# Performance work log

Hardware: AMD Instinct MI355X
Metric: run time of the kernel (lower is better)

## Reference

```python
import jax, jax.numpy as jnp
import numpy as np

STAGE_NUM = 5
BETA = 1.0
EPS = 1e-6


def _em_refine(cls, proto):
    # cls: [b, d]; proto: [k, d]. Matches torch einsum('bd,bkd->bk') with
    # batch-replicated prototypes == cls @ proto.T (no (b,k,d) materialization).
    p = proto
    for _ in range(STAGE_NUM):
        r = jax.nn.softmax(cls @ p.T, axis=1)          # [b, k]
        p = r.T @ cls                                   # [k, d]
        p = p / (jnp.linalg.norm(p, axis=1, keepdims=True) + EPS)
    return p


def setup_inputs() -> dict:
    key = jax.random.key(0)
    k1, k2 = jax.random.split(key)
    b, d, k = 8192, 1024, 512
    cls = jax.random.normal(k1, (b, d), dtype=jnp.float32)
    proto = jax.random.normal(k2, (k, d), dtype=jnp.float32)
    # __init__ normalizes prototypes to unit norm (with 1e-6 in denominator)
    proto = proto / (1e-6 + jnp.linalg.norm(proto, axis=1, keepdims=True))
    return {"cls": cls, "prototypes": proto}


def reference(cls, prototypes):
    # EM loop runs under torch.no_grad() -> stop_gradient here.
    new_proto = jax.lax.stop_gradient(_em_refine(cls, prototypes))  # [k, d]
    dot = cls @ new_proto.T                                          # [b, k]
    r = jax.nn.softmax(dot, axis=1)
    z_recon = r @ new_proto                                          # [b, d]
    z_out = BETA * z_recon + cls
    return (r, z_out)
```

## Files before the change

kernel.cpp:

```cpp
#include <hip/hip_runtime.h>

typedef short v8s __attribute__((ext_vector_type(8)));
typedef _Float16 v8h __attribute__((ext_vector_type(8)));
typedef float v4f __attribute__((ext_vector_type(4)));

typedef __attribute__((address_space(1))) const void* as1_void_cp;
typedef __attribute__((address_space(3))) void* as3_void_p;

__device__ __forceinline__ unsigned short f2bf(float x) {
  union { float f; unsigned int u; } v; v.f = x;
  unsigned int r = v.u + 0x7fffu + ((v.u >> 16) & 1u);
  return (unsigned short)(r >> 16);
}
__device__ __forceinline__ float bf2f(unsigned short h) {
  union { unsigned int u; float f; } v; v.u = ((unsigned int)h) << 16;
  return v.f;
}
__device__ __forceinline__ unsigned short f2h(float x) {
  _Float16 h = (_Float16)x;
  return __builtin_bit_cast(unsigned short, h);
}

struct B3 { int x, y, z; };
__device__ __forceinline__ B3 xcd_swizzle() {
  const int gx = gridDim.x, gy = gridDim.y;
  const int nwg = gx * gy * gridDim.z;
  int flat = blockIdx.x + gx * (blockIdx.y + gy * blockIdx.z);
  if ((nwg & 7) == 0) flat = (flat & 7) * (nwg >> 3) + (flat >> 3);
  B3 b;
  b.x = flat % gx;
  b.y = (flat / gx) % gy;
  b.z = flat / (gx * gy);
  return b;
}

template <bool ADD, bool F16>
__global__ __launch_bounds__(256) void gemm_bt(
    const unsigned short* __restrict__ A, const unsigned short* __restrict__ B,
    float* __restrict__ C, const float* __restrict__ Cadd,
    int N, int lda, int ldb, int klen, size_t csplit) {
  __shared__ __align__(16) unsigned short As[2][128 * 64];
  __shared__ __align__(16) unsigned short Bs[2][128 * 64];
  const int tid = threadIdx.x;
  const B3 bid = xcd_swizzle();
  const int bn = bid.x * 128, bm = bid.y * 128;
  const int k0 = bid.z * klen;
  float* Cp = C + (size_t)bid.z * csplit;

  const unsigned short* ag0 = A + (size_t)(bm + (tid >> 2)) * lda + ((tid & 3) << 3) + k0;
  const unsigned short* ag1 = ag0 + (size_t)64 * lda;
  const unsigned short* bg0 = B + (size_t)(bn + (tid >> 2)) * ldb + ((tid & 3) << 3) + k0;
  const unsigned short* bg1 = bg0 + (size_t)64 * ldb;

  const int lane = tid & 63;
  const int q = lane >> 4, m15 = lane & 15;
  const int w = tid >> 6;
  const int wr = (w >> 1) * 64, wc = (w & 1) * 64;

  v4f acc[4][4];
#pragma unroll
  for (int i = 0; i < 4; ++i)
#pragma unroll
    for (int j = 0; j < 4; ++j) acc[i][j] = 0.f;

  auto stage = [&](int kk, int b) {
    unsigned short* al = As[b] + tid * 8;
    unsigned short* bl = Bs[b] + tid * 8;
    __builtin_amdgcn_global_load_lds((as1_void_cp)(ag0 + kk), (as3_void_p)al, 16, 0, 0);
    __builtin_amdgcn_global_load_lds((as1_void_cp)(ag1 + kk), (as3_void_p)(al + 2048), 16, 0, 0);
    __builtin_amdgcn_global_load_lds((as1_void_cp)(ag0 + kk + 32), (as3_void_p)(al + 4096), 16, 0, 0);
    __builtin_amdgcn_global_load_lds((as1_void_cp)(ag1 + kk + 32), (as3_void_p)(al + 6144), 16, 0, 0);
    __builtin_amdgcn_global_load_lds((as1_void_cp)(bg0 + kk), (as3_void_p)bl, 16, 0, 0);
    __builtin_amdgcn_global_load_lds((as1_void_cp)(bg1 + kk), (as3_void_p)(bl + 2048), 16, 0, 0);
    __builtin_amdgcn_global_load_lds((as1_void_cp)(bg0 + kk + 32), (as3_void_p)(bl + 4096), 16, 0, 0);
    __builtin_amdgcn_global_load_lds((as1_void_cp)(bg1 + kk + 32), (as3_void_p)(bl + 6144), 16, 0, 0);
  };

  const int nt = klen >> 6;
  stage(0, 0);
  if (nt > 1) stage(64, 1);
  for (int t = 0; t < nt; ++t) {
    if (t + 1 < nt)
      asm volatile("s_waitcnt vmcnt(8)" ::: "memory");
    else
      asm volatile("s_waitcnt vmcnt(0)" ::: "memory");
    __builtin_amdgcn_s_barrier();
    const unsigned short* Ab = As[t & 1];
    const unsigned short* Bb = Bs[t & 1];
#pragma unroll
    for (int h = 0; h < 2; ++h) {
      v8s af[4], bf[4];
#pragma unroll
      for (int i = 0; i < 4; ++i)
        af[i] = *(const v8s*)(Ab + h * 4096 + (wr + i * 16 + m15) * 32 + q * 8);
#pragma unroll
      for (int j = 0; j < 4; ++j)
        bf[j] = *(const v8s*)(Bb + h * 4096 + (wc + j * 16 + m15) * 32 + q * 8);
#pragma unroll
      for (int i = 0; i < 4; ++i)
#pragma unroll
        for (int j = 0; j < 4; ++j) {
          if constexpr (F16)
            acc[i][j] = __builtin_amdgcn_mfma_f32_16x16x32_f16(
                __builtin_bit_cast(v8h, af[i]), __builtin_bit_cast(v8h, bf[j]), acc[i][j], 0, 0, 0);
          else
            acc[i][j] = __builtin_amdgcn_mfma_f32_16x16x32_bf16(af[i], bf[j], acc[i][j], 0, 0, 0);
        }
    }
    if (t + 2 < nt) {
      __builtin_amdgcn_s_barrier();
      stage((t + 2) << 6, t & 1);
    }
  }

#pragma unroll
  for (int i = 0; i < 4; ++i) {
#pragma unroll
    for (int j = 0; j < 4; ++j) {
      const int col = bn + wc + j * 16 + m15;
#pragma unroll
      for (int rr = 0; rr < 4; ++rr) {
        const int row = bm + wr + i * 16 + q * 4 + rr;
        const size_t idx = (size_t)row * N + col;
        float v = acc[i][j][rr];
        if (ADD) v += Cadd[idx];
        Cp[idx] = v;
      }
    }
  }
}

__global__ __launch_bounds__(256) void gemm_bt3(
    const unsigned short* __restrict__ Ah, const unsigned short* __restrict__ Al,
    const unsigned short* __restrict__ Bh, const unsigned short* __restrict__ Bl,
    float* __restrict__ C, int N, int lda, int ldb, int klen, size_t csplit) {
  __shared__ __align__(16) unsigned short Ash[2][128 * 32];
  __shared__ __align__(16) unsigned short Asl[2][128 * 32];
  __shared__ __align__(16) unsigned short Bsh[2][128 * 32];
  __shared__ __align__(16) unsigned short Bsl[2][128 * 32];
  const int tid = threadIdx.x;
  const B3 bid = xcd_swizzle();
  const int bn = bid.x * 128, bm = bid.y * 128;
  const int k0 = bid.z * klen;
  float* Cp = C + (size_t)bid.z * csplit;

  const size_t aoff = (size_t)(bm + (tid >> 2)) * lda + ((tid & 3) << 3) + k0;
  const size_t boff = (size_t)(bn + (tid >> 2)) * ldb + ((tid & 3) << 3) + k0;
  const unsigned short* agh0 = Ah + aoff;
  const unsigned short* agh1 = agh0 + (size_t)64 * lda;
  const unsigned short* agl0 = Al + aoff;
  const unsigned short* agl1 = agl0 + (size_t)64 * lda;
  const unsigned short* bgh0 = Bh + boff;
  const unsigned short* bgh1 = bgh0 + (size_t)64 * ldb;
  const unsigned short* bgl0 = Bl + boff;
  const unsigned short* bgl1 = bgl0 + (size_t)64 * ldb;

  const int lane = tid & 63;
  const int q = lane >> 4, m15 = lane & 15;
  const int w = tid >> 6;
  const int wr = (w >> 1) * 64, wc = (w & 1) * 64;

  v4f acc[4][4];
#pragma unroll
  for (int i = 0; i < 4; ++i)
#pragma unroll
    for (int j = 0; j < 4; ++j) acc[i][j] = 0.f;

  auto stage = [&](int kk, int b) {
    __builtin_amdgcn_global_load_lds((as1_void_cp)(agh0 + kk), (as3_void_p)(Ash[b] + tid * 8), 16, 0, 0);
    __builtin_amdgcn_global_load_lds((as1_void_cp)(agh1 + kk), (as3_void_p)(Ash[b] + 2048 + tid * 8), 16, 0, 0);
    __builtin_amdgcn_global_load_lds((as1_void_cp)(agl0 + kk), (as3_void_p)(Asl[b] + tid * 8), 16, 0, 0);
    __builtin_amdgcn_global_load_lds((as1_void_cp)(agl1 + kk), (as3_void_p)(Asl[b] + 2048 + tid * 8), 16, 0, 0);
    __builtin_amdgcn_global_load_lds((as1_void_cp)(bgh0 + kk), (as3_void_p)(Bsh[b] + tid * 8), 16, 0, 0);
    __builtin_amdgcn_global_load_lds((as1_void_cp)(bgh1 + kk), (as3_void_p)(Bsh[b] + 2048 + tid * 8), 16, 0, 0);
    __builtin_amdgcn_global_load_lds((as1_void_cp)(bgl0 + kk), (as3_void_p)(Bsl[b] + tid * 8), 16, 0, 0);
    __builtin_amdgcn_global_load_lds((as1_void_cp)(bgl1 + kk), (as3_void_p)(Bsl[b] + 2048 + tid * 8), 16, 0, 0);
  };

  const int nt = klen >> 5;
  stage(0, 0);
  if (nt > 1) stage(32, 1);
  for (int t = 0; t < nt; ++t) {
    if (t + 1 < nt)
      asm volatile("s_waitcnt vmcnt(8)" ::: "memory");
    else
      asm volatile("s_waitcnt vmcnt(0)" ::: "memory");
    __builtin_amdgcn_s_barrier();
    const int b = t & 1;
    v8s afh[4], afl[4], bfh[4], bfl[4];
#pragma unroll
    for (int i = 0; i < 4; ++i) {
      const int ro = (wr + i * 16 + m15) * 32 + q * 8;
      afh[i] = *(const v8s*)(Ash[b] + ro);
      afl[i] = *(const v8s*)(Asl[b] + ro);
    }
#pragma unroll
    for (int j = 0; j < 4; ++j) {
      const int ro = (wc + j * 16 + m15) * 32 + q * 8;
      bfh[j] = *(const v8s*)(Bsh[b] + ro);
      bfl[j] = *(const v8s*)(Bsl[b] + ro);
    }
#pragma unroll
    for (int i = 0; i < 4; ++i)
#pragma unroll
      for (int j = 0; j < 4; ++j) {
        acc[i][j] = __builtin_amdgcn_mfma_f32_16x16x32_bf16(afh[i], bfh[j], acc[i][j], 0, 0, 0);
        acc[i][j] = __builtin_amdgcn_mfma_f32_16x16x32_bf16(afh[i], bfl[j], acc[i][j], 0, 0, 0);
        acc[i][j] = __builtin_amdgcn_mfma_f32_16x16x32_bf16(afl[i], bfh[j], acc[i][j], 0, 0, 0);
      }
    if (t + 2 < nt) {
      __builtin_amdgcn_s_barrier();
      stage((t + 2) << 5, b);
    }
  }

#pragma unroll
  for (int i = 0; i < 4; ++i) {
#pragma unroll
    for (int j = 0; j < 4; ++j) {
      const int col = bn + wc + j * 16 + m15;
#pragma unroll
      for (int rr = 0; rr < 4; ++rr) {
        const int row = bm + wr + i * 16 + q * 4 + rr;
        Cp[(size_t)row * N + col] = acc[i][j][rr];
      }
    }
  }
}

__global__ __launch_bounds__(256) void cast_split_transpose_cls(
    const float* __restrict__ cls,
    unsigned short* __restrict__ ch, unsigned short* __restrict__ cl,
    unsigned short* __restrict__ cTh, unsigned short* __restrict__ cTl,
    unsigned short* __restrict__ cg, unsigned short* __restrict__ cTg) {
  __shared__ unsigned short th[64][72];
  __shared__ unsigned short tl[64][72];
  const int d0 = blockIdx.x * 64, b0 = blockIdx.y * 64;
  const int t = threadIdx.x;
#pragma unroll
  for (int i = 0; i < 4; ++i) {
    int flat = t + i * 256;
    int bl_ = flat >> 4;
    int dl = (flat & 15) << 2;
    float4 v = *(const float4*)(cls + (size_t)(b0 + bl_) * 1024 + d0 + dl);
    ushort4 h, l, g;
    h.x = f2bf(v.x); l.x = f2bf(v.x - bf2f(h.x)); g.x = f2h(bf2f(h.x) + bf2f(l.x));
    h.y = f2bf(v.y); l.y = f2bf(v.y - bf2f(h.y)); g.y = f2h(bf2f(h.y) + bf2f(l.y));
    h.z = f2bf(v.z); l.z = f2bf(v.z - bf2f(h.z)); g.z = f2h(bf2f(h.z) + bf2f(l.z));
    h.w = f2bf(v.w); l.w = f2bf(v.w - bf2f(h.w)); g.w = f2h(bf2f(h.w) + bf2f(l.w));
    *(ushort4*)(ch + (size_t)(b0 + bl_) * 1024 + d0 + dl) = h;
    *(ushort4*)(cl + (size_t)(b0 + bl_) * 1024 + d0 + dl) = l;
    *(ushort4*)(cg + (size_t)(b0 + bl_) * 1024 + d0 + dl) = g;
    th[bl_][dl] = h.x; th[bl_][dl + 1] = h.y; th[bl_][dl + 2] = h.z; th[bl_][dl + 3] = h.w;
    tl[bl_][dl] = l.x; tl[bl_][dl + 1] = l.y; tl[bl_][dl + 2] = l.z; tl[bl_][dl + 3] = l.w;
  }
  __syncthreads();
#pragma unroll
  for (int i = 0; i < 4; ++i) {
    int flat = t + i * 256;
    int dl = flat >> 4;
    int bl_ = (flat & 15) << 2;
    ushort4 h = make_ushort4(th[bl_][dl], th[bl_ + 1][dl], th[bl_ + 2][dl], th[bl_ + 3][dl]);
    ushort4 l = make_ushort4(tl[bl_][dl], tl[bl_ + 1][dl], tl[bl_ + 2][dl], tl[bl_ + 3][dl]);
    ushort4 g;
    g.x = f2h(bf2f(h.x) + bf2f(l.x));
    g.y = f2h(bf2f(h.y) + bf2f(l.y));
    g.z = f2h(bf2f(h.z) + bf2f(l.z));
    g.w = f2h(bf2f(h.w) + bf2f(l.w));
    *(ushort4*)(cTh + (size_t)(d0 + dl) * 8192 + b0 + bl_) = h;
    *(ushort4*)(cTl + (size_t)(d0 + dl) * 8192 + b0 + bl_) = l;
    *(ushort4*)(cTg + (size_t)(d0 + dl) * 8192 + b0 + bl_) = g;
  }
}

__global__ __launch_bounds__(256) void split_f32(const float* __restrict__ in,
                                                 unsigned short* __restrict__ hi,
                                                 unsigned short* __restrict__ lo) {
  const size_t i = (size_t)(blockIdx.x * blockDim.x + threadIdx.x) * 4;
  float4 v = *(const float4*)(in + i);
  ushort4 h, l;
  h.x = f2bf(v.x); l.x = f2bf(v.x - bf2f(h.x));
  h.y = f2bf(v.y); l.y = f2bf(v.y - bf2f(h.y));
  h.z = f2bf(v.z); l.z = f2bf(v.z - bf2f(h.z));
  h.w = f2bf(v.w); l.w = f2bf(v.w - bf2f(h.w));
  *(ushort4*)(hi + i) = h;
  *(ushort4*)(lo + i) = l;
}

template <bool HILO>
__global__ __launch_bounds__(512) void rowsoftmax_T(
    const float* __restrict__ SP0, const float* __restrict__ SP1,
    unsigned short* __restrict__ rTh, unsigned short* __restrict__ rTl) {
  __shared__ __align__(16) unsigned short th[32 * 520];
  __shared__ __align__(16) unsigned short tl[HILO ? 32 * 520 : 8];
  const int t = threadIdx.x;
  const int lane = t & 63, w = t >> 6;
  const int b0 = blockIdx.x * 32;
#pragma unroll
  for (int k = 0; k < 4; ++k) {
    const int bl = w * 4 + k;
    const int row = b0 + bl;
    const size_t off = (size_t)row * 512 + lane * 8;
    float4 v0 = *(const float4*)(SP0 + off);
    float4 v1 = *(const float4*)(SP0 + off + 4);
    float4 u0 = *(const float4*)(SP1 + off);
    float4 u1 = *(const float4*)(SP1 + off + 4);
    float e[8];
    e[0] = v0.x + u0.x; e[1] = v0.y + u0.y; e[2] = v0.z + u0.z; e[3] = v0.w + u0.w;
    e[4] = v1.x + u1.x; e[5] = v1.y + u1.y; e[6] = v1.z + u1.z; e[7] = v1.w + u1.w;
    float m = fmaxf(fmaxf(fmaxf(e[0], e[1]), fmaxf(e[2], e[3])),
                    fmaxf(fmaxf(e[4], e[5]), fmaxf(e[6], e[7])));
    for (int o = 32; o; o >>= 1) m = fmaxf(m, __shfl_xor(m, o));
    float s = 0.f;
#pragma unroll
    for (int i = 0; i < 8; ++i) { e[i] = __expf(e[i] - m); s += e[i]; }
    for (int o = 32; o; o >>= 1) s += __shfl_xor(s, o);
    const float inv = 1.f / s;
    unsigned short ph[8], pl[8];
#pragma unroll
    for (int i = 0; i < 8; ++i) {
      const float r = e[i] * inv;
      if constexpr (HILO) {
        ph[i] = f2bf(r);
        pl[i] = f2bf(r - bf2f(ph[i]));
      } else {
        ph[i] = f2h(r);
      }
    }
    *(v8s*)&th[bl * 520 + lane * 8] = *(v8s*)ph;
    if constexpr (HILO) *(v8s*)&tl[bl * 520 + lane * 8] = *(v8s*)pl;
  }
  __syncthreads();
  const int c = t;
  unsigned short uh[32];
#pragma unroll
  for (int b = 0; b < 32; ++b) uh[b] = th[b * 520 + c];
#pragma unroll
  for (int q = 0; q < 4; ++q)
    *(v8s*)(rTh + (size_t)c * 8192 + b0 + q * 8) = *(v8s*)&uh[q * 8];
  if constexpr (HILO) {
    unsigned short ul[32];
#pragma unroll
    for (int b = 0; b < 32; ++b) ul[b] = tl[b * 520 + c];
#pragma unroll
    for (int q = 0; q < 4; ++q)
      *(v8s*)(rTl + (size_t)c * 8192 + b0 + q * 8) = *(v8s*)&ul[q * 8];
  }
}

__global__ __launch_bounds__(256) void softmax_rows(const float* __restrict__ SP0,
                                                    const float* __restrict__ SP1,
                                                    float* __restrict__ r_out,
                                                    unsigned short* __restrict__ r_g) {
  const int w = threadIdx.x >> 6, lane = threadIdx.x & 63;
  const int row = blockIdx.x * 4 + w;
  const size_t off = (size_t)row * 512 + lane * 8;
  float4 v0 = *(const float4*)(SP0 + off);
  float4 v1 = *(const float4*)(SP0 + off + 4);
  float4 u0 = *(const float4*)(SP1 + off);
  float4 u1 = *(const float4*)(SP1 + off + 4);
  v0.x += u0.x; v0.y += u0.y; v0.z += u0.z; v0.w += u0.w;
  v1.x += u1.x; v1.y += u1.y; v1.z += u1.z; v1.w += u1.w;
  float m = fmaxf(fmaxf(fmaxf(v0.x, v0.y), fmaxf(v0.z, v0.w)),
                  fmaxf(fmaxf(v1.x, v1.y), fmaxf(v1.z, v1.w)));
  for (int off2 = 32; off2; off2 >>= 1) m = fmaxf(m, __shfl_xor(m, off2));
  float e0 = __expf(v0.x - m), e1 = __expf(v0.y - m), e2 = __expf(v0.z - m), e3 = __expf(v0.w - m);
  float e4 = __expf(v1.x - m), e5 = __expf(v1.y - m), e6 = __expf(v1.z - m), e7 = __expf(v1.w - m);
  float s = e0 + e1 + e2 + e3 + e4 + e5 + e6 + e7;
  for (int off2 = 32; off2; off2 >>= 1) s += __shfl_xor(s, off2);
  const float inv = 1.f / s;
  e0 *= inv; e1 *= inv; e2 *= inv; e3 *= inv; e4 *= inv; e5 *= inv; e6 *= inv; e7 *= inv;
  float* rp = r_out + off;
  *(float4*)rp = make_float4(e0, e1, e2, e3);
  *(float4*)(rp + 4) = make_float4(e4, e5, e6, e7);
  unsigned short* bp = r_g + off;
  *(ushort4*)bp = make_ushort4(f2h(e0), f2h(e1), f2h(e2), f2h(e3));
  *(ushort4*)(bp + 4) = make_ushort4(f2h(e4), f2h(e5), f2h(e6), f2h(e7));
}

__global__ __launch_bounds__(256) void reduce_normalize(const float* __restrict__ Pp,
                                                        unsigned short* __restrict__ pg,
                                                        unsigned short* __restrict__ pTg) {
  __shared__ float red[4];
  const int c = blockIdx.x, t = threadIdx.x;
  float ax = 0.f, ay = 0.f, az = 0.f, aw = 0.f;
#pragma unroll
  for (int s = 0; s < 16; ++s) {
    const float4 v = *(const float4*)(Pp + ((size_t)s * 512 + c) * 1024 + t * 4);
    ax += v.x; ay += v.y; az += v.z; aw += v.w;
  }
  float ss = ax * ax + ay * ay + az * az + aw * aw;
  for (int off = 32; off; off >>= 1) ss += __shfl_xor(ss, off);
  const int w = t >> 6, lane = t & 63;
  if (!lane) red[w] = ss;
  __syncthreads();
  const float tot = red[0] + red[1] + red[2] + red[3];
  const float scale = 1.f / (sqrtf(tot) + 1e-6f);
  ax *= scale; ay *= scale; az *= scale; aw *= scale;
  *(ushort4*)(pg + (size_t)c * 1024 + t * 4) =
      make_ushort4(f2h(ax), f2h(ay), f2h(az), f2h(aw));
  pTg[(size_t)(t * 4 + 0) * 512 + c] = f2h(ax);
  pTg[(size_t)(t * 4 + 1) * 512 + c] = f2h(ay);
  pTg[(size_t)(t * 4 + 2) * 512 + c] = f2h(az);
  pTg[(size_t)(t * 4 + 3) * 512 + c] = f2h(aw);
}

extern "C" void kernel_launch(void* const* d_in, const int* in_sizes, int n_in,
                              void* d_out, int out_size, void* d_ws, size_t ws_size,
                              hipStream_t stream) {
  const float* cls = (const float*)d_in[0];
  const float* proto = (const float*)d_in[1];
  float* out_r = (float*)d_out;
  float* out_z = out_r + (size_t)8192 * 512;

  char* w = (char*)d_ws;
  unsigned short* cls_h = (unsigned short*)w; w += (size_t)8192 * 1024 * 2;
  unsigned short* cls_l = (unsigned short*)w; w += (size_t)8192 * 1024 * 2;
  unsigned short* clsT_h = (unsigned short*)w; w += (size_t)1024 * 8192 * 2;
  unsigned short* clsT_l = (unsigned short*)w; w += (size_t)1024 * 8192 * 2;
  unsigned short* cls_g = (unsigned short*)w; w += (size_t)8192 * 1024 * 2;
  unsigned short* clsT_g = (unsigned short*)w; w += (size_t)1024 * 8192 * 2;
  unsigned short* p_h = (unsigned short*)w; w += (size_t)512 * 1024 * 2;
  unsigned short* p_l = (unsigned short*)w; w += (size_t)512 * 1024 * 2;
  unsigned short* p_g = (unsigned short*)w; w += (size_t)512 * 1024 * 2;
  unsigned short* pT_g = (unsigned short*)w; w += (size_t)1024 * 512 * 2;
  unsigned short* rT_h = (unsigned short*)w; w += (size_t)512 * 8192 * 2;
  unsigned short* rT_l = (unsigned short*)w; w += (size_t)512 * 8192 * 2;
  float* SP = (float*)w;
  float* SP1 = SP + (size_t)8192 * 512;

  cast_split_transpose_cls<<<dim3(16, 128), 256, 0, stream>>>(
      cls, cls_h, cls_l, clsT_h, clsT_l, cls_g, clsT_g);
  split_f32<<<512, 256, 0, stream>>>(proto, p_h, p_l);

  gemm_bt3<<<dim3(4, 64, 2), 256, 0, stream>>>(cls_h, cls_l, p_h, p_l, SP,
                                               512, 1024, 1024, 512,
                                               (size_t)8192 * 512);
  rowsoftmax_T<true><<<256, 512, 0, stream>>>(SP, SP1, rT_h, rT_l);
  gemm_bt3<<<dim3(8, 4, 16), 256, 0, stream>>>(rT_h, rT_l, clsT_h, clsT_l, SP,
                                               1024, 8192, 8192, 512,
                                               (size_t)512 * 1024);
  reduce_normalize<<<512, 256, 0, stream>>>(SP, p_g, pT_g);

  for (int it = 0; it < 4; ++it) {
    gemm_bt<false, true><<<dim3(4, 64, 2), 256, 0, stream>>>(cls_g, p_g, SP, nullptr,
                                                             512, 1024, 1024, 512,
                                                             (size_t)8192 * 512);
    rowsoftmax_T<false><<<256, 512, 0, stream>>>(SP, SP1, rT_h, nullptr);
    gemm_bt<false, true><<<dim3(8, 4, 16), 256, 0, stream>>>(rT_h, clsT_g, SP, nullptr,
                                                             1024, 8192, 8192, 512,
                                                             (size_t)512 * 1024);
    reduce_normalize<<<512, 256, 0, stream>>>(SP, p_g, pT_g);
  }

  gemm_bt<false, true><<<dim3(4, 64, 2), 256, 0, stream>>>(cls_g, p_g, SP, nullptr,
                                                           512, 1024, 1024, 512,
                                                           (size_t)8192 * 512);
  softmax_rows<<<2048, 256, 0, stream>>>(SP, SP1, out_r, rT_h);
  gemm_bt<true, true><<<dim3(8, 64, 1), 256, 0, stream>>>(rT_h, pT_g, out_z, cls,
                                                          1024, 512, 512, 512, 0);
}
```

Before: 446.1 us.

## Fuse score GEMM with row softmax and transpose into one kernel

Adds a kernel in which each block computes a 32-row by 512-column score tile with f16 MFMA and then applies the row softmax in registers. It writes the transposed f16 responsibilities directly, or in the final pass the fp32 r output plus the row-major f16 copy. This replaces the split-K score GEMM, its fp32 partial-sum round trip and the separate softmax kernel in the last five EM stages. The risk is that only 256 blocks run, with a large LDS footprint (about 136 KB), which limits occupancy and parallelism compared with the old split-K launch.

Result: slower. 471.2 us (+5.6%).

```diff
diff --git a/kernel.cpp b/kernel.cpp
--- a/kernel.cpp
+++ b/kernel.cpp
@@ -225,6 +225,173 @@
         Cp[(size_t)row * N + col] = acc[i][j][rr];
       }
     }
+  }
+}
+
+template <bool FINAL>
+__global__ __launch_bounds__(256) void s_softmax_fused(
+    const unsigned short* __restrict__ A,
+    const unsigned short* __restrict__ B,
+    unsigned short* __restrict__ rT,
+    float* __restrict__ r_out,
+    unsigned short* __restrict__ r_row) {
+  __shared__ __align__(16) unsigned short As[2][32 * 64];
+  __shared__ __align__(16) unsigned short Bs[2][512 * 64];
+  __shared__ float redm[4][32];
+  __shared__ float reds[4][32];
+  const int tid = threadIdx.x;
+  const int lane = tid & 63;
+  const int wv = tid >> 6;
+  const int q = lane >> 4, m15 = lane & 15;
+  const int wc = wv * 128;
+  const int b0 = blockIdx.x * 32;
+
+  const int srow = tid >> 3, scol = (tid & 7) << 3;
+  const unsigned short* ag = A + (size_t)(b0 + srow) * 1024 + scol;
+  const unsigned short* bg = B + (size_t)srow * 1024 + scol;
+
+  auto stage = [&](int kk, int b) {
+    __builtin_amdgcn_global_load_lds((as1_void_cp)(ag + kk), (as3_void_p)(As[b] + tid * 8), 16, 0, 0);
+#pragma unroll
+    for (int s = 0; s < 16; ++s)
+      __builtin_amdgcn_global_load_lds((as1_void_cp)(bg + (size_t)s * 32 * 1024 + kk),
+                                       (as3_void_p)(Bs[b] + s * 2048 + tid * 8), 16, 0, 0);
+  };
+
+  v4f acc[2][8];
+#pragma unroll
+  for (int i = 0; i < 2; ++i)
+#pragma unroll
+    for (int j = 0; j < 8; ++j) acc[i][j] = 0.f;
+
+  stage(0, 0);
+  stage(64, 1);
+  for (int t = 0; t < 16; ++t) {
+    if (t < 15)
+      asm volatile("s_waitcnt vmcnt(17)" ::: "memory");
+    else
+      asm volatile("s_waitcnt vmcnt(0)" ::: "memory");
+    __builtin_amdgcn_s_barrier();
+    const unsigned short* Ab = As[t & 1];
+    const unsigned short* Bb = Bs[t & 1];
+#pragma unroll
+    for (int h = 0; h < 2; ++h) {
+      v8s af[2], bf[8];
+#pragma unroll
+      for (int i = 0; i < 2; ++i)
+        af[i] = *(const v8s*)(Ab + (i * 16 + m15) * 64 + h * 32 + q * 8);
+#pragma unroll
+      for (int j = 0; j < 8; ++j)
+        bf[j] = *(const v8s*)(Bb + (wc + j * 16 + m15) * 64 + h * 32 + q * 8);
+#pragma unroll
+      for (int i = 0; i < 2; ++i)
+#pragma unroll
+        for (int j = 0; j < 8; ++j)
+          acc[i][j] = __builtin_amdgcn_mfma_f32_16x16x32_f16(
+              __builtin_bit_cast(v8h, af[i]), __builtin_bit_cast(v8h, bf[j]), acc[i][j], 0, 0, 0);
+    }
+    if (t + 2 < 16) {
+      __builtin_amdgcn_s_barrier();
+      stage((t + 2) << 6, t & 1);
+    }
+  }
+
+  float mx[2][4];
+#pragma unroll
+  for (int i = 0; i < 2; ++i)
+#pragma unroll
+    for (int rr = 0; rr < 4; ++rr) {
+      float m = acc[i][0][rr];
+#pragma unroll
+      for (int j = 1; j < 8; ++j) m = fmaxf(m, acc[i][j][rr]);
+      m = fmaxf(m, __shfl_xor(m, 1));
+      m = fmaxf(m, __shfl_xor(m, 2));
+      m = fmaxf(m, __shfl_xor(m, 4));
+      m = fmaxf(m, __shfl_xor(m, 8));
+      mx[i][rr] = m;
+    }
+  if (m15 == 0) {
+#pragma unroll
+    for (int i = 0; i < 2; ++i)
+#pragma unroll
+      for (int rr = 0; rr < 4; ++rr) redm[wv][i * 16 + q * 4 + rr] = mx[i][rr];
+  }
+  __syncthreads();
+#pragma unroll
+  for (int i = 0; i < 2; ++i)
+#pragma unroll
+    for (int rr = 0; rr < 4; ++rr) {
+      const int row = i * 16 + q * 4 + rr;
+      mx[i][rr] = fmaxf(fmaxf(redm[0][row], redm[1][row]),
+                        fmaxf(redm[2][row], redm[3][row]));
+    }
+
+  float sm[2][4];
+#pragma unroll
+  for (int i = 0; i < 2; ++i)
+#pragma unroll
+    for (int rr = 0; rr < 4; ++rr) {
+      float s = 0.f;
+#pragma unroll
+      for (int j = 0; j < 8; ++j) {
+        const float e = __expf(acc[i][j][rr] - mx[i][rr]);
+        acc[i][j][rr] = e;
+        s += e;
+      }
+      s += __shfl_xor(s, 1);
+      s += __shfl_xor(s, 2);
+      s += __shfl_xor(s, 4);
+      s += __shfl_xor(s, 8);
+      sm[i][rr] = s;
+    }
+  if (m15 == 0) {
+#pragma unroll
+    for (int i = 0; i < 2; ++i)
+#pragma unroll
+      for (int rr = 0; rr < 4; ++rr) reds[wv][i * 16 + q * 4 + rr] = sm[i][rr];
+  }
+  __syncthreads();
+#pragma unroll
+  for (int i = 0; i < 2; ++i)
+#pragma unroll
+    for (int rr = 0; rr < 4; ++rr) {
+      const int row = i * 16 + q * 4 + rr;
+      sm[i][rr] = 1.f / (reds[0][row] + reds[1][row] + reds[2][row] + reds[3][row]);
+    }
+
+  unsigned short* th = (unsigned short*)&Bs[0][0];
+#pragma unroll
+  for (int i = 0; i < 2; ++i)
+#pragma unroll
+    for (int j = 0; j < 8; ++j)
+#pragma unroll
+      for (int rr = 0; rr < 4; ++rr) {
+        const float v = acc[i][j][rr] * sm[i][rr];
+        const int row = i * 16 + q * 4 + rr;
+        const int col = wc + j * 16 + m15;
+        th[row * 520 + col] = f2h(v);
+        if constexpr (FINAL) r_out[(size_t)(b0 + row) * 512 + col] = v;
+      }
+  __syncthreads();
+
+  if constexpr (!FINAL) {
+#pragma unroll
+    for (int cc = 0; cc < 2; ++cc) {
+      const int c = tid + cc * 256;
+      unsigned short uh[32];
+#pragma unroll
+      for (int b = 0; b < 32; ++b) uh[b] = th[b * 520 + c];
+#pragma unroll
+      for (int u = 0; u < 4; ++u)
+        *(v8s*)(rT + (size_t)c * 8192 + b0 + u * 8) = *(v8s*)&uh[u * 8];
+    }
+  } else {
+    const int row = tid >> 3;
+    const int c0 = (tid & 7) * 64;
+#pragma unroll
+    for (int u = 0; u < 8; ++u)
+      *(v8s*)(r_row + (size_t)(b0 + row) * 512 + c0 + u * 8) =
+          *(const v8s*)&th[row * 520 + c0 + u * 8];
   }
 }
 
@@ -348,36 +515,6 @@
   }
 }
 
-__global__ __launch_bounds__(256) void softmax_rows(const float* __restrict__ SP0,
-                                                    const float* __restrict__ SP1,
-                                                    float* __restrict__ r_out,
-                                                    unsigned short* __restrict__ r_g) {
-  const int w = threadIdx.x >> 6, lane = threadIdx.x & 63;
-  const int row = blockIdx.x * 4 + w;
-  const size_t off = (size_t)row * 512 + lane * 8;
-  float4 v0 = *(const float4*)(SP0 + off);
-  float4 v1 = *(const float4*)(SP0 + off + 4);
-  float4 u0 = *(const float4*)(SP1 + off);
-  float4 u1 = *(const float4*)(SP1 + off + 4);
-  v0.x += u0.x; v0.y += u0.y; v0.z += u0.z; v0.w += u0.w;
-  v1.x += u1.x; v1.y += u1.y; v1.z += u1.z; v1.w += u1.w;
-  float m = fmaxf(fmaxf(fmaxf(v0.x, v0.y), fmaxf(v0.z, v0.w)),
-                  fmaxf(fmaxf(v1.x, v1.y), fmaxf(v1.z, v1.w)));
-  for (int off2 = 32; off2; off2 >>= 1) m = fmaxf(m, __shfl_xor(m, off2));
-  float e0 = __expf(v0.x - m), e1 = __expf(v0.y - m), e2 = __expf(v0.z - m), e3 = __expf(v0.w - m);
-  float e4 = __expf(v1.x - m), e5 = __expf(v1.y - m), e6 = __expf(v1.z - m), e7 = __expf(v1.w - m);
-  float s = e0 + e1 + e2 + e3 + e4 + e5 + e6 + e7;
-  for (int off2 = 32; off2; off2 >>= 1) s += __shfl_xor(s, off2);
-  const float inv = 1.f / s;
-  e0 *= inv; e1 *= inv; e2 *= inv; e3 *= inv; e4 *= inv; e5 *= inv; e6 *= inv; e7 *= inv;
-  float* rp = r_out + off;
-  *(float4*)rp = make_float4(e0, e1, e2, e3);
-  *(float4*)(rp + 4) = make_float4(e4, e5, e6, e7);
-  unsigned short* bp = r_g + off;
-  *(ushort4*)bp = make_ushort4(f2h(e0), f2h(e1), f2h(e2), f2h(e3));
-  *(ushort4*)(bp + 4) = make_ushort4(f2h(e4), f2h(e5), f2h(e6), f2h(e7));
-}
-
 __global__ __launch_bounds__(256) void reduce_normalize(const float* __restrict__ Pp,
                                                         unsigned short* __restrict__ pg,
                                                         unsigned short* __restrict__ pTg) {
@@ -443,20 +580,14 @@
   reduce_normalize<<<512, 256, 0, stream>>>(SP, p_g, pT_g);
 
   for (int it = 0; it < 4; ++it) {
-    gemm_bt<false, true><<<dim3(4, 64, 2), 256, 0, stream>>>(cls_g, p_g, SP, nullptr,
-                                                             512, 1024, 1024, 512,
-                                                             (size_t)8192 * 512);
-    rowsoftmax_T<false><<<256, 512, 0, stream>>>(SP, SP1, rT_h, nullptr);
+    s_softmax_fused<false><<<256, 256, 0, stream>>>(cls_g, p_g, rT_h, nullptr, nullptr);
     gemm_bt<false, true><<<dim3(8, 4, 16), 256, 0, stream>>>(rT_h, clsT_g, SP, nullptr,
                                                              1024, 8192, 8192, 512,
                                                              (size_t)512 * 1024);
     reduce_normalize<<<512, 256, 0, stream>>>(SP, p_g, pT_g);
   }
 
-  gemm_bt<false, true><<<dim3(4, 64, 2), 256, 0, stream>>>(cls_g, p_g, SP, nullptr,
-                                                           512, 1024, 1024, 512,
-                                                           (size_t)8192 * 512);
-  softmax_rows<<<2048, 256, 0, stream>>>(SP, SP1, out_r, rT_h);
+  s_softmax_fused<true><<<256, 256, 0, stream>>>(cls_g, p_g, nullptr, out_r, rT_h);
   gemm_bt<true, true><<<dim3(8, 64, 1), 256, 0, stream>>>(rT_h, pT_g, out_z, cls,
                                                           1024, 512, 512, 512, 0);
 }
```

## Add 64x128 K64 fp16 GEMM and drop split-K in EM iterations

Applied to the files above, without the earlier changes.

Adds gemm_bt64, an fp16 MFMA GEMM with a 64x128 output tile and a 64-wide K stage, double-buffered through global_load_lds. In the four low-precision EM iterations and the final score GEMM, it replaces the 128x128 split-K=2 score GEMM with a 64-row tile and no split. The update GEMM drops from split-K 16 to 8. This removes the second partial-sum buffer read in the softmax kernels and halves the partial reads in reduce_normalize, at the cost of smaller tiles with lower per-block reuse.

Measured after the change: 436.9 us. 2.1% less time.

```diff
diff --git a/kernel.cpp b/kernel.cpp
--- a/kernel.cpp
+++ b/kernel.cpp
@@ -125,6 +125,90 @@
         float v = acc[i][j][rr];
         if (ADD) v += Cadd[idx];
         Cp[idx] = v;
+      }
+    }
+  }
+}
+
+__global__ __launch_bounds__(256) void gemm_bt64(
+    const unsigned short* __restrict__ A, const unsigned short* __restrict__ B,
+    float* __restrict__ C, int N, int lda, int ldb, int klen, size_t csplit) {
+  __shared__ __align__(16) unsigned short As[2][64 * 64];
+  __shared__ __align__(16) unsigned short Bs[2][128 * 64];
+  const int tid = threadIdx.x;
+  const B3 bid = xcd_swizzle();
+  const int bn = bid.x * 128, bm = bid.y * 64;
+  const int k0 = bid.z * klen;
+  float* Cp = C + (size_t)bid.z * csplit;
+
+  const unsigned short* ag0 = A + (size_t)(bm + (tid >> 2)) * lda + ((tid & 3) << 3) + k0;
+  const unsigned short* bg0 = B + (size_t)(bn + (tid >> 2)) * ldb + ((tid & 3) << 3) + k0;
+  const unsigned short* bg1 = bg0 + (size_t)64 * ldb;
+
+  const int lane = tid & 63;
+  const int q = lane >> 4, m15 = lane & 15;
+  const int w = tid >> 6;
+  const int wr = (w >> 1) * 32, wc = (w & 1) * 64;
+
+  v4f acc[2][4];
+#pragma unroll
+  for (int i = 0; i < 2; ++i)
+#pragma unroll
+    for (int j = 0; j < 4; ++j) acc[i][j] = 0.f;
+
+  auto stage = [&](int kk, int b) {
+    unsigned short* al = As[b] + tid * 8;
+    unsigned short* bl = Bs[b] + tid * 8;
+    __builtin_amdgcn_global_load_lds((as1_void_cp)(ag0 + kk), (as3_void_p)al, 16, 0, 0);
+    __builtin_amdgcn_global_load_lds((as1_void_cp)(ag0 + kk + 32), (as3_void_p)(al + 2048), 16, 0, 0);
+    __builtin_amdgcn_global_load_lds((as1_void_cp)(bg0 + kk), (as3_void_p)bl, 16, 0, 0);
+    __builtin_amdgcn_global_load_lds((as1_void_cp)(bg1 + kk), (as3_void_p)(bl + 2048), 16, 0, 0);
+    __builtin_amdgcn_global_load_lds((as1_void_cp)(bg0 + kk + 32), (as3_void_p)(bl + 4096), 16, 0, 0);
+    __builtin_amdgcn_global_load_lds((as1_void_cp)(bg1 + kk + 32), (as3_void_p)(bl + 6144), 16, 0, 0);
+  };
+
+  const int nt = klen >> 6;
+  stage(0, 0);
+  if (nt > 1) stage(64, 1);
+  for (int t = 0; t < nt; ++t) {
+    if (t + 1 < nt)
+      asm volatile("s_waitcnt vmcnt(6)" ::: "memory");
+    else
+      asm volatile("s_waitcnt vmcnt(0)" ::: "memory");
+    __builtin_amdgcn_s_barrier();
+    const unsigned short* Ab = As[t & 1];
+    const unsigned short* Bb = Bs[t & 1];
+#pragma unroll
+    for (int h = 0; h < 2; ++h) {
+      v8s af[2], bf[4];
+#pragma unroll
+      for (int i = 0; i < 2; ++i)
+        af[i] = *(const v8s*)(Ab + h * 2048 + (wr + i * 16 + m15) * 32 + q * 8);
+#pragma unroll
+      for (int j = 0; j < 4; ++j)
+        bf[j] = *(const v8s*)(Bb + h * 4096 + (wc + j * 16 + m15) * 32 + q * 8);
+#pragma unroll
+      for (int i = 0; i < 2; ++i)
+#pragma unroll
+        for (int j = 0; j < 4; ++j)
+          acc[i][j] = __builtin_amdgcn_mfma_f32_16x16x32_f16(
+              __builtin_bit_cast(v8h, af[i]), __builtin_bit_cast(v8h, bf[j]), acc[i][j], 0, 0, 0);
+    }
+    if (t + 2 < nt) {
+      __builtin_amdgcn_s_barrier();
+      stage((t + 2) << 6, t & 1);
+    }
+  }
+
+#pragma unroll
+  for (int i = 0; i < 2; ++i) {
+#pragma unroll
+    for (int j = 0; j < 4; ++j) {
+      const int col = bn + wc + j * 16 + m15;
+#pragma unroll
+      for (int rr = 0; rr < 4; ++rr) {
+        const int row = bm + wr + i * 16 + q * 4 + rr;
+        Cp[(size_t)row * N + col] = acc[i][j][rr];
       }
     }
   }
@@ -287,7 +371,7 @@
   *(ushort4*)(lo + i) = l;
 }
 
-template <bool HILO>
+template <bool HILO, bool SPLIT>
 __global__ __launch_bounds__(512) void rowsoftmax_T(
     const float* __restrict__ SP0, const float* __restrict__ SP1,
     unsigned short* __restrict__ rTh, unsigned short* __restrict__ rTl) {
@@ -303,11 +387,15 @@
     const size_t off = (size_t)row * 512 + lane * 8;
     float4 v0 = *(const float4*)(SP0 + off);
     float4 v1 = *(const float4*)(SP0 + off + 4);
-    float4 u0 = *(const float4*)(SP1 + off);
-    float4 u1 = *(const float4*)(SP1 + off + 4);
     float e[8];
-    e[0] = v0.x + u0.x; e[1] = v0.y + u0.y; e[2] = v0.z + u0.z; e[3] = v0.w + u0.w;
-    e[4] = v1.x + u1.x; e[5] = v1.y + u1.y; e[6] = v1.z + u1.z; e[7] = v1.w + u1.w;
+    e[0] = v0.x; e[1] = v0.y; e[2] = v0.z; e[3] = v0.w;
+    e[4] = v1.x; e[5] = v1.y; e[6] = v1.z; e[7] = v1.w;
+    if constexpr (SPLIT) {
+      float4 u0 = *(const float4*)(SP1 + off);
+      float4 u1 = *(const float4*)(SP1 + off + 4);
+      e[0] += u0.x; e[1] += u0.y; e[2] += u0.z; e[3] += u0.w;
+      e[4] += u1.x; e[5] += u1.y; e[6] += u1.z; e[7] += u1.w;
+    }
     float m = fmaxf(fmaxf(fmaxf(e[0], e[1]), fmaxf(e[2], e[3])),
                     fmaxf(fmaxf(e[4], e[5]), fmaxf(e[6], e[7])));
     for (int o = 32; o; o >>= 1) m = fmaxf(m, __shfl_xor(m, o));
@@ -349,7 +437,6 @@
 }
 
 __global__ __launch_bounds__(256) void softmax_rows(const float* __restrict__ SP0,
-                                                    const float* __restrict__ SP1,
                                                     float* __restrict__ r_out,
                                                     unsigned short* __restrict__ r_g) {
   const int w = threadIdx.x >> 6, lane = threadIdx.x & 63;
@@ -357,10 +444,6 @@
   const size_t off = (size_t)row * 512 + lane * 8;
   float4 v0 = *(const float4*)(SP0 + off);
   float4 v1 = *(const float4*)(SP0 + off + 4);
-  float4 u0 = *(const float4*)(SP1 + off);
-  float4 u1 = *(const float4*)(SP1 + off + 4);
-  v0.x += u0.x; v0.y += u0.y; v0.z += u0.z; v0.w += u0.w;
-  v1.x += u1.x; v1.y += u1.y; v1.z += u1.z; v1.w += u1.w;
   float m = fmaxf(fmaxf(fmaxf(v0.x, v0.y), fmaxf(v0.z, v0.w)),
                   fmaxf(fmaxf(v1.x, v1.y), fmaxf(v1.z, v1.w)));
   for (int off2 = 32; off2; off2 >>= 1) m = fmaxf(m, __shfl_xor(m, off2));
@@ -378,6 +461,7 @@
   *(ushort4*)(bp + 4) = make_ushort4(f2h(e4), f2h(e5), f2h(e6), f2h(e7));
 }
 
+template <int NS>
 __global__ __launch_bounds__(256) void reduce_normalize(const float* __restrict__ Pp,
                                                         unsigned short* __restrict__ pg,
                                                         unsigned short* __restrict__ pTg) {
@@ -385,7 +469,7 @@
   const int c = blockIdx.x, t = threadIdx.x;
   float ax = 0.f, ay = 0.f, az = 0.f, aw = 0.f;
 #pragma unroll
-  for (int s = 0; s < 16; ++s) {
+  for (int s = 0; s < NS; ++s) {
     const float4 v = *(const float4*)(Pp + ((size_t)s * 512 + c) * 1024 + t * 4);
     ax += v.x; ay += v.y; az += v.z; aw += v.w;
   }
@@ -436,27 +520,25 @@
   gemm_bt3<<<dim3(4, 64, 2), 256, 0, stream>>>(cls_h, cls_l, p_h, p_l, SP,
                                                512, 1024, 1024, 512,
                                                (size_t)8192 * 512);
-  rowsoftmax_T<true><<<256, 512, 0, stream>>>(SP, SP1, rT_h, rT_l);
+  rowsoftmax_T<true, true><<<256, 512, 0, stream>>>(SP, SP1, rT_h, rT_l);
   gemm_bt3<<<dim3(8, 4, 16), 256, 0, stream>>>(rT_h, rT_l, clsT_h, clsT_l, SP,
                                                1024, 8192, 8192, 512,
                                                (size_t)512 * 1024);
-  reduce_normalize<<<512, 256, 0, stream>>>(SP, p_g, pT_g);
+  reduce_normalize<16><<<512, 256, 0, stream>>>(SP, p_g, pT_g);
 
   for (int it = 0; it < 4; ++it) {
-    gemm_bt<false, true><<<dim3(4, 64, 2), 256, 0, stream>>>(cls_g, p_g, SP, nullptr,
-                                                             512, 1024, 1024, 512,
-                                                             (size_t)8192 * 512);
-    rowsoftmax_T<false><<<256, 512, 0, stream>>>(SP, SP1, rT_h, nullptr);
-    gemm_bt<false, true><<<dim3(8, 4, 16), 256, 0, stream>>>(rT_h, clsT_g, SP, nullptr,
-                                                             1024, 8192, 8192, 512,
-                                                             (size_t)512 * 1024);
-    reduce_normalize<<<512, 256, 0, stream>>>(SP, p_g, pT_g);
-  }
-
-  gemm_bt<false, true><<<dim3(4, 64, 2), 256, 0, stream>>>(cls_g, p_g, SP, nullptr,
-                                                           512, 1024, 1024, 512,
-                                                           (size_t)8192 * 512);
-  softmax_rows<<<2048, 256, 0, stream>>>(SP, SP1, out_r, rT_h);
+    gemm_bt64<<<dim3(4, 128, 1), 256, 0, stream>>>(cls_g, p_g, SP,
+                                                   512, 1024, 1024, 1024, 0);
+    rowsoftmax_T<false, false><<<256, 512, 0, stream>>>(SP, nullptr, rT_h, nullptr);
+    gemm_bt64<<<dim3(8, 8, 8), 256, 0, stream>>>(rT_h, clsT_g, SP,
+                                                 1024, 8192, 8192, 1024,
+                                                 (size_t)512 * 1024);
+    reduce_normalize<8><<<512, 256, 0, stream>>>(SP, p_g, pT_g);
+  }
+
+  gemm_bt64<<<dim3(4, 128, 1), 256, 0, stream>>>(cls_g, p_g, SP,
+                                                 512, 1024, 1024, 1024, 0);
+  softmax_rows<<<2048, 256, 0, stream>>>(SP, out_r, rT_h);
   gemm_bt<true, true><<<dim3(8, 64, 1), 256, 0, stream>>>(rT_h, pT_g, out_z, cls,
                                                           1024, 512, 512, 512, 0);
 }
```
